# Kernel optimization log

Measured on AMD Instinct MI355X. Metric: run time of the kernel, lower is better.

## Reference

```python
import jax, jax.numpy as jnp
import numpy as np

# AFD = permute -> VSSBlock (LN + SS2D Mamba selective scan, residual) -> permute
#       -> x + SAFM(ChannelLayerNorm(x))
C = 64        # in_channels (d_model)
DI = 128      # d_inner = expand(2) * d_model
N = 16        # d_state
R = 4         # dt_rank = ceil(64/16)
K = 4         # scan directions
LN_EPS = 1e-5
CN_EPS = 1e-6
B_, H_, W_ = 8, 64, 64


def setup_inputs() -> dict:
    key = jax.random.key(0)
    ks = jax.random.split(key, 16)
    f = lambda k, s, sc=0.02: jax.random.normal(k, s, jnp.float32) * sc
    return {
        'x': jax.random.normal(ks[0], (B_, C, H_, W_), jnp.float32),
        # VSSBlock ln_1
        'ln1_g': jnp.ones((C,), jnp.float32),
        'ln1_b': jnp.zeros((C,), jnp.float32),
        # SS2D
        'in_proj_w': f(ks[1], (2 * DI, C)),
        'in_proj_b': jnp.zeros((2 * DI,), jnp.float32),
        'conv_w': f(ks[2], (DI, 3, 3)),          # depthwise 3x3
        'conv_b': jnp.zeros((DI,), jnp.float32),
        'xproj_w': f(ks[3], (K, R + 2 * N, DI)),
        'dtproj_w': f(ks[4], (K, DI, R), 0.1),
        'dtproj_b': f(ks[5], (K, DI), 0.1),
        'A_logs': jnp.tile(jnp.log(jnp.arange(1, N + 1, dtype=jnp.float32)), (K * DI, 1)),
        'Ds': jnp.ones((K * DI,), jnp.float32),
        'outnorm_g': jnp.ones((DI,), jnp.float32),
        'outnorm_b': jnp.zeros((DI,), jnp.float32),
        'outproj_w': f(ks[6], (C, DI)),
        'outproj_b': jnp.zeros((C,), jnp.float32),
        # SAFM
        'mfr_w': f(ks[7], (4, C // 4, 3, 3)),    # 4 depthwise 3x3 convs
        'mfr_b': jnp.zeros((4, C // 4), jnp.float32),
        'aggr_w': f(ks[8], (C, C)),              # 1x1 conv
        'aggr_b': jnp.zeros((C,), jnp.float32),
        # channel LayerNorm (SAFMN-style, channels_first)
        'cn_g': jnp.ones((C,), jnp.float32),
        'cn_b': jnp.zeros((C,), jnp.float32),
    }


def _ln(x, g, b, eps):
    u = jnp.mean(x, -1, keepdims=True)
    v = jnp.mean((x - u) ** 2, -1, keepdims=True)
    return (x - u) * jax.lax.rsqrt(v + eps) * g + b


def _channel_ln(x, g, b):  # x: (B,C,H,W), normalize over C
    u = jnp.mean(x, 1, keepdims=True)
    v = jnp.mean((x - u) ** 2, 1, keepdims=True)
    return (x - u) * jax.lax.rsqrt(v + CN_EPS) * g[None, :, None, None] + b[None, :, None, None]


def _dwconv3(x, w, b):  # depthwise 3x3, pad 1. x: (B,C,H,W), w: (C,3,3)
    y = jax.lax.conv_general_dilated(x, w[:, None], (1, 1), 'SAME',
        dimension_numbers=('NCHW', 'OIHW', 'NCHW'), feature_group_count=x.shape[1])
    return y + b[None, :, None, None]


def _selective_scan(xs, dts, A, Bs, Cs, D):
    # xs,dts:(B,K,C,L)  Bs,Cs:(B,K,N,L)  A:(K,C,N)  D:(K,C)
    u = jnp.moveaxis(xs, -1, 0)
    dt = jnp.moveaxis(dts, -1, 0)
    Bl = jnp.moveaxis(Bs, -1, 0)
    Cl = jnp.moveaxis(Cs, -1, 0)

    def step(h, inp):
        u_t, dt_t, B_t, C_t = inp
        h = h * jnp.exp(dt_t[..., None] * A) + dt_t[..., None] * B_t[:, :, None, :] * u_t[..., None]
        return h, jnp.einsum('bkcn,bkn->bkc', h, C_t)

    h0 = jnp.zeros(u.shape[1:] + (A.shape[-1],), u.dtype)
    _, ys = jax.lax.scan(step, h0, (u, dt, Bl, Cl))
    return jnp.moveaxis(ys, 0, -1) + D[None, :, :, None] * xs


def _ss2d(x, in_proj_w, in_proj_b, conv_w, conv_b, xproj_w, dtproj_w, dtproj_b,
          A_logs, Ds, outnorm_g, outnorm_b, outproj_w, outproj_b):
    B, H, W, _ = x.shape
    L = H * W
    xz = jnp.einsum('bhwc,dc->bhwd', x, in_proj_w) + in_proj_b
    xi, z = jnp.split(xz, 2, axis=-1)
    xc = jnp.transpose(xi, (0, 3, 1, 2))                      # (B,DI,H,W)
    xc = jax.nn.silu(_dwconv3(xc, conv_w, conv_b))
    # 4-directional unfold: row-major, col-major, and their reverses
    x_flat = xc.reshape(B, DI, L)
    x_t = jnp.transpose(xc, (0, 1, 3, 2)).reshape(B, DI, L)
    x_hwwh = jnp.stack([x_flat, x_t], axis=1)                 # (B,2,DI,L)
    xs = jnp.concatenate([x_hwwh, jnp.flip(x_hwwh, axis=-1)], axis=1)  # (B,4,DI,L)
    x_dbl = jnp.einsum('bkdl,kcd->bkcl', xs, xproj_w)
    dts, Bs, Cs = jnp.split(x_dbl, [R, R + N], axis=2)
    dts = jnp.einsum('bkrl,kdr->bkdl', dts, dtproj_w)
    dts = jax.nn.softplus(dts + dtproj_b[None, :, :, None])
    A = -jnp.exp(A_logs).reshape(K, DI, N)
    out_y = _selective_scan(xs, dts, A, Bs, Cs, Ds.reshape(K, DI))  # (B,4,DI,L)
    inv = jnp.flip(out_y[:, 2:4], axis=-1)
    wh = jnp.transpose(out_y[:, 1].reshape(B, DI, W, H), (0, 1, 3, 2)).reshape(B, DI, L)
    invwh = jnp.transpose(inv[:, 1].reshape(B, DI, W, H), (0, 1, 3, 2)).reshape(B, DI, L)
    y = out_y[:, 0] + inv[:, 0] + wh + invwh                  # (B,DI,L)
    y = jnp.transpose(y, (0, 2, 1)).reshape(B, H, W, DI)
    y = _ln(y, outnorm_g, outnorm_b, LN_EPS) * jax.nn.silu(z)
    return jnp.einsum('bhwd,cd->bhwc', y, outproj_w) + outproj_b


def _safm(x, mfr_w, mfr_b, aggr_w, aggr_b):
    parts = jnp.split(x, 4, axis=1)
    outs = []
    for i in range(4):
        s = parts[i]
        k = 2 ** i
        if i > 0:  # adaptive max pool to (H/k, W/k) == maxpool k,k
            s = jax.lax.reduce_window(s, -jnp.inf, jax.lax.max, (1, 1, k, k), (1, 1, k, k), 'VALID')
        s = _dwconv3(s, mfr_w[i], mfr_b[i])
        if i > 0:  # nearest upsample back
            s = jnp.repeat(jnp.repeat(s, k, axis=2), k, axis=3)
        outs.append(s)
    out = jnp.concatenate(outs, axis=1)
    out = jnp.einsum('bchw,oc->bohw', out, aggr_w) + aggr_b[None, :, None, None]
    return jax.nn.gelu(out, approximate=False) * x


def reference(x, ln1_g, ln1_b, in_proj_w, in_proj_b, conv_w, conv_b, xproj_w,
              dtproj_w, dtproj_b, A_logs, Ds, outnorm_g, outnorm_b, outproj_w,
              outproj_b, mfr_w, mfr_b, aggr_w, aggr_b, cn_g, cn_b):
    xh = jnp.transpose(x, (0, 2, 3, 1))                       # NCHW -> NHWC
    xh = xh + _ss2d(_ln(xh, ln1_g, ln1_b, LN_EPS), in_proj_w, in_proj_b, conv_w,
                    conv_b, xproj_w, dtproj_w, dtproj_b, A_logs, Ds,
                    outnorm_g, outnorm_b, outproj_w, outproj_b)
    xo = jnp.transpose(xh, (0, 3, 1, 2))                      # NHWC -> NCHW
    return xo + _safm(_channel_ln(xo, cn_g, cn_b), mfr_w, mfr_b, aggr_w, aggr_b)
```

## Files before the change

### kernel.cpp

```cpp
#include <hip/hip_runtime.h>
#include <hip/hip_bf16.h>

#define BB 8
#define CC 64
#define HH 64
#define WW 64
#define LL 4096
#define DI 128
#define KK 4
#define NN 16
#define RR 4
#define XD 36
#define GG 64
#define TT 64

__device__ __forceinline__ float softplusf(float x){
    return fmaxf(x, 0.f) + __logf(1.f + __expf(-fabsf(x)));
}
__device__ __forceinline__ int p_of(int k, int t){
    int tt = (k & 2) ? (LL - 1 - t) : t;
    return (k & 1) ? ((tt & 63) * 64 + (tt >> 6)) : tt;
}

template<int CTRL>
__device__ __forceinline__ float dpp_xadd(float v){
    int t = __builtin_amdgcn_update_dpp(0, __float_as_int(v), CTRL, 0xF, 0xF, true);
    return v + __int_as_float(t);
}

__global__ __launch_bounds__(256) void k1_ln_inproj(
    const float* __restrict__ x,
    const float* __restrict__ ln1_g,
    const float* __restrict__ ln1_b,
    const float* __restrict__ ipw,
    const float* __restrict__ ipb,
    float* __restrict__ xi, float* __restrict__ zs)
{
    int bid = blockIdx.x;
    int b = bid >> 6, p0 = (bid & 63)*64;
    int tid = threadIdx.x;

    __shared__ float xs[64*65];
    __shared__ float lnxT[64*68];
    __shared__ float wT[16*260];
    __shared__ float gb[128];
    __shared__ float bias[256];
    __shared__ float red[512];
    __shared__ float mv[128];

    if (tid < 128) gb[tid] = (tid < 64) ? ln1_g[tid] : ln1_b[tid - 64];
    bias[tid] = ipb[tid];

    #pragma unroll
    for (int it = 0; it < 4; it++){
        int i = tid + it*256;
        int c = i >> 4, pq = i & 15;
        float4 v = *(const float4*)(x + ((size_t)(b*CC + c))*LL + p0 + pq*4);
        xs[(pq*4+0)*65 + c] = v.x;
        xs[(pq*4+1)*65 + c] = v.y;
        xs[(pq*4+2)*65 + c] = v.z;
        xs[(pq*4+3)*65 + c] = v.w;
    }
    __syncthreads();

    {
        int pix = tid >> 2, q = tid & 3;
        float s = 0.f, sq = 0.f;
        #pragma unroll
        for (int cc = 0; cc < 16; cc++){
            float v = xs[pix*65 + q*16 + cc];
            s += v; sq = fmaf(v, v, sq);
        }
        red[tid*2] = s; red[tid*2+1] = sq;
    }
    __syncthreads();
    if (tid < 64){
        float s = red[tid*8] + red[tid*8+2] + red[tid*8+4] + red[tid*8+6];
        float sq = red[tid*8+1] + red[tid*8+3] + red[tid*8+5] + red[tid*8+7];
        float mean = s * (1.f/64.f);
        float var  = sq * (1.f/64.f) - mean*mean;
        mv[tid*2] = mean; mv[tid*2+1] = rsqrtf(var + 1e-5f);
    }
    __syncthreads();
    {
        int pix = tid >> 2, q = tid & 3;
        float mean = mv[pix*2], rstd = mv[pix*2+1];
        #pragma unroll
        for (int cc = 0; cc < 16; cc++){
            int c = q*16 + cc;
            float v = (xs[pix*65 + c] - mean)*rstd*gb[c] + gb[64+c];
            lnxT[c*68 + pix] = v;
        }
    }

    int pt = tid >> 4, ot = tid & 15;
    float acc[16][4];
    #pragma unroll
    for (int j = 0; j < 16; j++)
        #pragma unroll
        for (int i2 = 0; i2 < 4; i2++) acc[j][i2] = 0.f;

    for (int kc = 0; kc < 4; kc++){
        __syncthreads();
        #pragma unroll
        for (int it = 0; it < 4; it++){
            int i = tid + it*256;
            int d = i >> 2, jq = i & 3;
            float4 wv = *(const float4*)(ipw + d*64 + kc*16 + jq*4);
            wT[(jq*4+0)*260 + d] = wv.x;
            wT[(jq*4+1)*260 + d] = wv.y;
            wT[(jq*4+2)*260 + d] = wv.z;
            wT[(jq*4+3)*260 + d] = wv.w;
        }
        __syncthreads();
        #pragma unroll
        for (int k = 0; k < 16; k++){
            float4 rv = *(const float4*)(lnxT + (kc*16 + k)*68 + pt*4);
            #pragma unroll
            for (int g = 0; g < 4; g++){
                float4 wv = *(const float4*)(wT + k*260 + g*64 + ot*4);
                acc[g*4+0][0] = fmaf(wv.x, rv.x, acc[g*4+0][0]);
                acc[g*4+0][1] = fmaf(wv.x, rv.y, acc[g*4+0][1]);
                acc[g*4+0][2] = fmaf(wv.x, rv.z, acc[g*4+0][2]);
                acc[g*4+0][3] = fmaf(wv.x, rv.w, acc[g*4+0][3]);
                acc[g*4+1][0] = fmaf(wv.y, rv.x, acc[g*4+1][0]);
                acc[g*4+1][1] = fmaf(wv.y, rv.y, acc[g*4+1][1]);
                acc[g*4+1][2] = fmaf(wv.y, rv.z, acc[g*4+1][2]);
                acc[g*4+1][3] = fmaf(wv.y, rv.w, acc[g*4+1][3]);
                acc[g*4+2][0] = fmaf(wv.z, rv.x, acc[g*4+2][0]);
                acc[g*4+2][1] = fmaf(wv.z, rv.y, acc[g*4+2][1]);
                acc[g*4+2][2] = fmaf(wv.z, rv.z, acc[g*4+2][2]);
                acc[g*4+2][3] = fmaf(wv.z, rv.w, acc[g*4+2][3]);
                acc[g*4+3][0] = fmaf(wv.w, rv.x, acc[g*4+3][0]);
                acc[g*4+3][1] = fmaf(wv.w, rv.y, acc[g*4+3][1]);
                acc[g*4+3][2] = fmaf(wv.w, rv.z, acc[g*4+3][2]);
                acc[g*4+3][3] = fmaf(wv.w, rv.w, acc[g*4+3][3]);
            }
        }
    }

    #pragma unroll
    for (int i2 = 0; i2 < 4; i2++){
        size_t prow = ((size_t)(b*LL) + p0 + pt*4 + i2);
        #pragma unroll
        for (int g = 0; g < 4; g++){
            int dbase = g*64 + ot*4;
            float4 v;
            v.x = acc[g*4+0][i2] + bias[dbase+0];
            v.y = acc[g*4+1][i2] + bias[dbase+1];
            v.z = acc[g*4+2][i2] + bias[dbase+2];
            v.w = acc[g*4+3][i2] + bias[dbase+3];
            if (g < 2){
                *(float4*)(xi + prow*DI + dbase) = v;
            } else {
                v.x = v.x / (1.f + __expf(-v.x));
                v.y = v.y / (1.f + __expf(-v.y));
                v.z = v.z / (1.f + __expf(-v.z));
                v.w = v.w / (1.f + __expf(-v.w));
                *(float4*)(zs + prow*DI + dbase - 128) = v;
            }
        }
    }
}

__global__ __launch_bounds__(256) void k2_dwconv(
    const float* __restrict__ xi,
    const float* __restrict__ cw,
    const float* __restrict__ cb,
    float* __restrict__ xc)
{
    int idx = blockIdx.x*256 + threadIdx.x;
    int d = idx & 127;
    int g = idx >> 7;
    int p0 = (g & 1023) * 4;
    int b = g >> 10;
    int h = p0 >> 6, w0 = p0 & 63;
    float wt[9];
    #pragma unroll
    for (int j = 0; j < 9; j++) wt[j] = cw[d*9 + j];
    float bv = cb[d];
    float acc[4] = {bv, bv, bv, bv};
    #pragma unroll
    for (int ky = 0; ky < 3; ky++){
        int hh = h + ky - 1;
        if ((unsigned)hh >= 64u) continue;
        const float* row = xi + ((size_t)(b*LL) + hh*64)*DI + d;
        float v0 = (w0 > 0)  ? row[(w0-1)*DI] : 0.f;
        float v1 = row[(w0+0)*DI];
        float v2 = row[(w0+1)*DI];
        float v3 = row[(w0+2)*DI];
        float v4 = row[(w0+3)*DI];
        float v5 = (w0 < 60) ? row[(w0+4)*DI] : 0.f;
        float wa = wt[ky*3], wbv = wt[ky*3+1], wc = wt[ky*3+2];
        acc[0] = fmaf(v0, wa, fmaf(v1, wbv, fmaf(v2, wc, acc[0])));
        acc[1] = fmaf(v1, wa, fmaf(v2, wbv, fmaf(v3, wc, acc[1])));
        acc[2] = fmaf(v2, wa, fmaf(v3, wbv, fmaf(v4, wc, acc[2])));
        acc[3] = fmaf(v3, wa, fmaf(v4, wbv, fmaf(v5, wc, acc[3])));
    }
    #pragma unroll
    for (int i = 0; i < 4; i++){
        float a = acc[i];
        float sg = 1.f / (1.f + __expf(-a));
        xc[((size_t)(b*LL) + p0 + i)*DI + d] = a * sg;
    }
}

__global__ __launch_bounds__(256) void k3_xdbl(
    const float* __restrict__ xc,
    const float* __restrict__ xpw,
    float* __restrict__ xdbl)
{
    int bid = blockIdx.x;
    int b = bid >> 6, ptile = bid & 63;
    int tid = threadIdx.x;
    int ot = tid & 15;
    int pt = tid >> 4;

    __shared__ float r[64*132];
    __shared__ float wT[32*192];

    const float* xcb = xc + ((size_t)(b*LL) + ptile*64)*DI;
    for (int i = tid; i < 2048; i += 256){
        int pix = i >> 5, kq = i & 31;
        float4 v = *(const float4*)(xcb + pix*128 + kq*4);
        *(float4*)(r + pix*132 + kq*4) = v;
    }

    float acc[9][4];
    #pragma unroll
    for (int j = 0; j < 9; j++)
        #pragma unroll
        for (int i2 = 0; i2 < 4; i2++) acc[j][i2] = 0.f;

    for (int kc = 0; kc < 4; kc++){
        __syncthreads();
        int k0 = kc*32;
        for (int i = tid; i < 1152; i += 256){
            int cl = i >> 3, jq = i & 7;
            float4 wv = *(const float4*)(xpw + cl*128 + k0 + jq*4);
            int o = (cl*456) >> 12;
            int j = cl - o*9;
            wT[(jq*4+0)*192 + o*12 + j] = wv.x;
            wT[(jq*4+1)*192 + o*12 + j] = wv.y;
            wT[(jq*4+2)*192 + o*12 + j] = wv.z;
            wT[(jq*4+3)*192 + o*12 + j] = wv.w;
        }
        __syncthreads();
        const float* rbase = r + (pt*4)*132 + k0;
        #pragma unroll 4
        for (int k = 0; k < 32; k++){
            float4 wa = *(const float4*)(wT + k*192 + ot*12);
            float4 wb = *(const float4*)(wT + k*192 + ot*12 + 4);
            float w8 = wT[k*192 + ot*12 + 8];
            float rv0 = rbase[k];
            float rv1 = rbase[132 + k];
            float rv2 = rbase[264 + k];
            float rv3 = rbase[396 + k];
            float wv[9] = {wa.x, wa.y, wa.z, wa.w, wb.x, wb.y, wb.z, wb.w, w8};
            float rv[4] = {rv0, rv1, rv2, rv3};
            #pragma unroll
            for (int j = 0; j < 9; j++)
                #pragma unroll
                for (int i2 = 0; i2 < 4; i2++)
                    acc[j][i2] = fmaf(wv[j], rv[i2], acc[j][i2]);
        }
    }

    int kd = ot >> 2;
    int cbase = (ot & 3)*9;
    size_t obase = ((size_t)(b*KK + kd))*LL;
    #pragma unroll
    for (int i2 = 0; i2 < 4; i2++){
        int p = ptile*64 + pt*4 + i2;
        int tT = (p & 63)*64 + (p >> 6);
        int t = (kd == 0) ? p : (kd == 1) ? tT : (kd == 2) ? (4095 - p) : (4095 - tT);
        float* dst = xdbl + (obase + t)*XD + cbase;
        #pragma unroll
        for (int j = 0; j < 9; j++) dst[j] = acc[j][i2];
    }
}

__global__ __launch_bounds__(128, 4) void k4a_local(
    const float* __restrict__ xc, const float* __restrict__ xdbl,
    const float* __restrict__ dtw, const float* __restrict__ dtb,
    const float* __restrict__ A_logs,
    float* __restrict__ Pbuf, float* __restrict__ Hbuf)
{
    int bid = blockIdx.x;
    int cc = bid & 63, k = (bid >> 6) & 3, b = bid >> 8;
    int d = threadIdx.x;
    int kd = k*DI + d;
    float4 wv4 = *(const float4*)(dtw + kd*4);
    float bias = dtb[kd];
    float An[16];
    bool fast = true;
    {
        const float4* al = (const float4*)(A_logs + kd*16);
        #pragma unroll
        for (int i = 0; i < 4; i++){
            float4 a = al[i];
            An[i*4+0] = -__expf(a.x); An[i*4+1] = -__expf(a.y);
            An[i*4+2] = -__expf(a.z); An[i*4+3] = -__expf(a.w);
        }
        #pragma unroll
        for (int n = 0; n < 16; n++)
            fast = fast && (fabsf(An[n] + (float)(n+1)) < 1e-3f*(float)(n+1));
    }
    __shared__ float sraw[TT*XD];
    const float* src = xdbl + ((size_t)(b*KK + k)*LL + cc*TT)*XD;
    for (int i = threadIdx.x; i < TT*XD/4; i += 128)
        ((float4*)sraw)[i] = ((const float4*)src)[i];
    __syncthreads();

    const float* xcb = xc + (size_t)b*LL*DI;
    float h[16];
    #pragma unroll
    for (int i = 0; i < 16; i++) h[i] = 0.f;
    float Sdt = 0.f;

    if (fast){
        for (int t = 0; t < TT; t++){
            const float* rp = sraw + t*XD;
            float4 xr = *(const float4*)rp;
            float dtr = fmaf(xr.x, wv4.x, fmaf(xr.y, wv4.y, fmaf(xr.z, wv4.z, fmaf(xr.w, wv4.w, bias))));
            float dt = softplusf(dtr);
            Sdt += dt;
            int p = p_of(k, cc*TT + t);
            float u = xcb[(size_t)p*DI + d];
            float du = dt * u;
            float4 B0 = *(const float4*)(rp + 4);
            float4 B1 = *(const float4*)(rp + 8);
            float4 B2 = *(const float4*)(rp + 12);
            float4 B3 = *(const float4*)(rp + 16);
            float Bv[16] = {B0.x,B0.y,B0.z,B0.w, B1.x,B1.y,B1.z,B1.w,
                            B2.x,B2.y,B2.z,B2.w, B3.x,B3.y,B3.z,B3.w};
            float e1 = exp2f(-1.44269504f * dt);
            float e = e1;
            h[0] = fmaf(h[0], e, du*Bv[0]);
            #pragma unroll
            for (int i = 1; i < 16; i++){
                e *= e1;
                h[i] = fmaf(h[i], e, du*Bv[i]);
            }
        }
        size_t ob = ((size_t)bid)*2048 + d*16;
        float P1 = exp2f(-1.44269504f * Sdt);
        float P = P1;
        Pbuf[ob] = P; Hbuf[ob] = h[0];
        #pragma unroll
        for (int i = 1; i < 16; i++){
            P *= P1;
            Pbuf[ob + i] = P;
            Hbuf[ob + i] = h[i];
        }
    } else {
        float An2[16];
        #pragma unroll
        for (int i = 0; i < 16; i++) An2[i] = An[i] * 1.44269504f;
        for (int t = 0; t < TT; t++){
            const float* rp = sraw + t*XD;
            float4 xr = *(const float4*)rp;
            float dtr = fmaf(xr.x, wv4.x, fmaf(xr.y, wv4.y, fmaf(xr.z, wv4.z, fmaf(xr.w, wv4.w, bias))));
            float dt = softplusf(dtr);
            Sdt += dt;
            int p = p_of(k, cc*TT + t);
            float u = xcb[(size_t)p*DI + d];
            float du = dt * u;
            float4 B0 = *(const float4*)(rp + 4);
            float4 B1 = *(const float4*)(rp + 8);
            float4 B2 = *(const float4*)(rp + 12);
            float4 B3 = *(const float4*)(rp + 16);
            float Bv[16] = {B0.x,B0.y,B0.z,B0.w, B1.x,B1.y,B1.z,B1.w,
                            B2.x,B2.y,B2.z,B2.w, B3.x,B3.y,B3.z,B3.w};
            #pragma unroll
            for (int i = 0; i < 16; i++)
                h[i] = fmaf(h[i], exp2f(dt*An2[i]), du*Bv[i]);
        }
        size_t ob = ((size_t)bid)*2048 + d*16;
        #pragma unroll
        for (int i = 0; i < 16; i++){
            Pbuf[ob + i] = exp2f(An2[i] * Sdt);
            Hbuf[ob + i] = h[i];
        }
    }
}

__global__ __launch_bounds__(256) void k4b_prop(
    const float* __restrict__ Pbuf, const float* __restrict__ Hbuf,
    float* __restrict__ hin_buf)
{
    int chain = blockIdx.x*256 + threadIdx.x;
    int bk = chain >> 11, s = chain & 2047;
    float hin = 0.f;
    for (int c = 0; c < GG; c++){
        size_t idx = ((size_t)(bk*GG + c))*2048 + s;
        hin_buf[idx] = hin;
        hin = fmaf(Pbuf[idx], hin, Hbuf[idx]);
    }
}

__global__ __launch_bounds__(128, 4) void k4c_emit(
    const float* __restrict__ xc, const float* __restrict__ xdbl,
    const float* __restrict__ dtw, const float* __restrict__ dtb,
    const float* __restrict__ A_logs, const float* __restrict__ Ds,
    const float* __restrict__ hin_buf,
    float* __restrict__ y)
{
    int bid = blockIdx.x;
    int cc = bid & 63, k = (bid >> 6) & 3, b = bid >> 8;
    int d = threadIdx.x;
    int kd = k*DI + d;
    float4 wv4 = *(const float4*)(dtw + kd*4);
    float bias = dtb[kd];
    float Dv = Ds[kd];
    float An[16];
    bool fast = true;
    {
        const float4* al = (const float4*)(A_logs + kd*16);
        #pragma unroll
        for (int i = 0; i < 4; i++){
            float4 a = al[i];
            An[i*4+0] = -__expf(a.x); An[i*4+1] = -__expf(a.y);
            An[i*4+2] = -__expf(a.z); An[i*4+3] = -__expf(a.w);
        }
        #pragma unroll
        for (int n = 0; n < 16; n++)
            fast = fast && (fabsf(An[n] + (float)(n+1)) < 1e-3f*(float)(n+1));
    }
    __shared__ float sraw[TT*XD];
    const float* src = xdbl + ((size_t)(b*KK + k)*LL + cc*TT)*XD;
    for (int i = threadIdx.x; i < TT*XD/4; i += 128)
        ((float4*)sraw)[i] = ((const float4*)src)[i];
    __syncthreads();

    const float* xcb = xc + (size_t)b*LL*DI;
    float* yb = y + (size_t)b*LL*DI;
    float h[16];
    {
        const float4* hi = (const float4*)(hin_buf + ((size_t)bid)*2048 + d*16);
        #pragma unroll
        for (int i = 0; i < 4; i++){
            float4 a = hi[i];
            h[i*4+0] = a.x; h[i*4+1] = a.y; h[i*4+2] = a.z; h[i*4+3] = a.w;
        }
    }

    if (fast){
        for (int t = 0; t < TT; t++){
            const float* rp = sraw + t*XD;
            float4 xr = *(const float4*)rp;
            float dtr = fmaf(xr.x, wv4.x, fmaf(xr.y, wv4.y, fmaf(xr.z, wv4.z, fmaf(xr.w, wv4.w, bias))));
            float dt = softplusf(dtr);
            int p = p_of(k, cc*TT + t);
            float u = xcb[(size_t)p*DI + d];
            float du = dt * u;
            float4 B0 = *(const float4*)(rp + 4);
            float4 B1 = *(const float4*)(rp + 8);
            float4 B2 = *(const float4*)(rp + 12);
            float4 B3 = *(const float4*)(rp + 16);
            float Bv[16] = {B0.x,B0.y,B0.z,B0.w, B1.x,B1.y,B1.z,B1.w,
                            B2.x,B2.y,B2.z,B2.w, B3.x,B3.y,B3.z,B3.w};
            float4 C0 = *(const float4*)(rp + 20);
            float4 C1 = *(const float4*)(rp + 24);
            float4 C2 = *(const float4*)(rp + 28);
            float4 C3 = *(const float4*)(rp + 32);
            float Cv[16] = {C0.x,C0.y,C0.z,C0.w, C1.x,C1.y,C1.z,C1.w,
                            C2.x,C2.y,C2.z,C2.w, C3.x,C3.y,C3.z,C3.w};
            float yv = Dv * u;
            float e1 = exp2f(-1.44269504f * dt);
            float e = e1;
            h[0] = fmaf(h[0], e, du*Bv[0]);
            yv = fmaf(h[0], Cv[0], yv);
            #pragma unroll
            for (int i = 1; i < 16; i++){
                e *= e1;
                h[i] = fmaf(h[i], e, du*Bv[i]);
                yv = fmaf(h[i], Cv[i], yv);
            }
            atomicAdd(&yb[(size_t)p*DI + d], yv);
        }
    } else {
        float An2[16];
        #pragma unroll
        for (int i = 0; i < 16; i++) An2[i] = An[i] * 1.44269504f;
        for (int t = 0; t < TT; t++){
            const float* rp = sraw + t*XD;
            float4 xr = *(const float4*)rp;
            float dtr = fmaf(xr.x, wv4.x, fmaf(xr.y, wv4.y, fmaf(xr.z, wv4.z, fmaf(xr.w, wv4.w, bias))));
            float dt = softplusf(dtr);
            int p = p_of(k, cc*TT + t);
            float u = xcb[(size_t)p*DI + d];
            float du = dt * u;
            float4 B0 = *(const float4*)(rp + 4);
            float4 B1 = *(const float4*)(rp + 8);
            float4 B2 = *(const float4*)(rp + 12);
            float4 B3 = *(const float4*)(rp + 16);
            float Bv[16] = {B0.x,B0.y,B0.z,B0.w, B1.x,B1.y,B1.z,B1.w,
                            B2.x,B2.y,B2.z,B2.w, B3.x,B3.y,B3.z,B3.w};
            float4 C0 = *(const float4*)(rp + 20);
            float4 C1 = *(const float4*)(rp + 24);
            float4 C2 = *(const float4*)(rp + 28);
            float4 C3 = *(const float4*)(rp + 32);
            float Cv[16] = {C0.x,C0.y,C0.z,C0.w, C1.x,C1.y,C1.z,C1.w,
                            C2.x,C2.y,C2.z,C2.w, C3.x,C3.y,C3.z,C3.w};
            float yv = Dv * u;
            #pragma unroll
            for (int i = 0; i < 16; i++){
                h[i] = fmaf(h[i], exp2f(dt*An2[i]), du*Bv[i]);
                yv = fmaf(h[i], Cv[i], yv);
            }
            atomicAdd(&yb[(size_t)p*DI + d], yv);
        }
    }
}

__global__ __launch_bounds__(256) void k4_scan(
    const float* __restrict__ xc, const float* __restrict__ xdbl,
    const float* __restrict__ dtw, const float* __restrict__ dtb,
    const float* __restrict__ A_logs, const float* __restrict__ Ds,
    float* __restrict__ y)
{
    int bid = blockIdx.x;
    int b = bid >> 5, k = (bid >> 3) & 3, grp = bid & 7;
    int d0 = grp * 16;
    int tid = threadIdx.x;
    int wv = tid >> 6, lane = tid & 63, n = lane & 15, j = lane >> 4;
    int ch = wv*4 + j;
    int d = d0 + ch;
    int kd = k*DI + d;
    float An = -__expf(A_logs[kd*NN + n]);
    int ch_s = tid & 15;
    int kds = k*DI + d0 + ch_s;
    float w0s = dtw[kds*4+0], w1s = dtw[kds*4+1], w2s = dtw[kds*4+2], w3s = dtw[kds*4+3];
    float bs  = dtb[kds];
    float Dvs = Ds[kds];
    __shared__ float sraw[64*XD];
    __shared__ float sdd[64*16*2];
    __shared__ float sdy[64*17];
    const float* xdbase = xdbl + (size_t)(b*KK + k)*LL*XD;
    const float* xcb = xc + (size_t)b*LL*DI;
    float* yb = y + (size_t)b*LL*DI;
    float h = 0.f;
    for (int cc = 0; cc < 64; cc++){
        __syncthreads();
        const float* src = xdbase + (size_t)cc*64*XD;
        for (int i2 = tid; i2 < 576; i2 += 256)
            ((float4*)sraw)[i2] = ((const float4*)src)[i2];
        #pragma unroll
        for (int it = 0; it < 4; it++){
            int idx = tid + it*256;
            int t = idx >> 4;
            int pu = p_of(k, cc*64 + t);
            float u = xcb[(size_t)pu*DI + d0 + ch_s];
            float4 xr = *(const float4*)(src + t*XD);
            float dtr = fmaf(xr.x, w0s, fmaf(xr.y, w1s, fmaf(xr.z, w2s, fmaf(xr.w, w3s, bs))));
            float dt = softplusf(dtr);
            sdd[idx*2]     = dt;
            sdd[idx*2 + 1] = dt*u;
            sdy[t*17 + ch_s] = Dvs * u;
        }
        __syncthreads();
        #pragma unroll
        for (int tg = 0; tg < 4; tg++){
            float myv = 0.f;
            #pragma unroll
            for (int it = 0; it < 16; it++){
                int t = tg*16 + it;
                float dt = sdd[(t*16 + ch)*2];
                float du = sdd[(t*16 + ch)*2 + 1];
                float Bn = sraw[t*XD + 4 + n];
                float Cn = sraw[t*XD + 20 + n];
                float e = __expf(dt * An);
                h = fmaf(h, e, du * Bn);
                float yv = h * Cn;
                yv = dpp_xadd<0xB1>(yv);
                yv = dpp_xadd<0x4E>(yv);
                yv = dpp_xadd<0x141>(yv);
                yv = dpp_xadd<0x140>(yv);
                if (it == n) myv = yv;
            }
            int t = tg*16 + n;
            float yt = myv + sdy[t*17 + ch];
            int p = p_of(k, cc*64 + t);
            atomicAdd(&yb[(size_t)p*DI + d], yt);
        }
    }
}

__global__ __launch_bounds__(256) void k5_out(
    const float* __restrict__ y, const float* __restrict__ zs,
    const float* __restrict__ on_g, const float* __restrict__ on_b,
    const float* __restrict__ opw,
    const float* __restrict__ opb,
    const float* __restrict__ x,
    const float* __restrict__ cn_g, const float* __restrict__ cn_b,
    float* __restrict__ xo, float* __restrict__ cl)
{
    int bid = blockIdx.x;
    int b = bid >> 6, p0 = (bid & 63)*64;
    int tid = threadIdx.x;

    __shared__ float vT[128*68];
    __shared__ float wT[128*68];
    __shared__ float gb[256];
    __shared__ float ob[64];
    __shared__ float cgb[128];
    __shared__ float red[2048];
    __shared__ float mv[128];

    gb[tid] = (tid < 128) ? on_g[tid] : on_b[tid - 128];
    if (tid < 64) ob[tid] = opb[tid];
    if (tid >= 128 && tid < 256) cgb[tid-128] = (tid < 192) ? cn_g[tid-128] : cn_b[tid-192];

    #pragma unroll
    for (int it = 0; it < 8; it++){
        int i = tid + it*256;
        int c = i >> 5, jq = i & 31;
        float4 wv = *(const float4*)(opw + c*128 + jq*4);
        wT[(jq*4+0)*68 + c] = wv.x;
        wT[(jq*4+1)*68 + c] = wv.y;
        wT[(jq*4+2)*68 + c] = wv.z;
        wT[(jq*4+3)*68 + c] = wv.w;
    }

    int pix = tid >> 2, q = tid & 3;
    size_t base = ((size_t)(b*LL) + p0 + pix)*DI + q*32;
    float yv[32];
    {
        const float4* y4 = (const float4*)(y + base);
        float s = 0.f, sq = 0.f;
        #pragma unroll
        for (int i = 0; i < 8; i++){
            float4 a = y4[i];
            yv[i*4+0] = a.x; yv[i*4+1] = a.y; yv[i*4+2] = a.z; yv[i*4+3] = a.w;
            s += a.x + a.y + a.z + a.w;
            sq = fmaf(a.x,a.x, fmaf(a.y,a.y, fmaf(a.z,a.z, fmaf(a.w,a.w, sq))));
        }
        red[tid*2] = s; red[tid*2+1] = sq;
    }
    __syncthreads();
    if (tid < 64){
        float s = red[tid*8] + red[tid*8+2] + red[tid*8+4] + red[tid*8+6];
        float sq = red[tid*8+1] + red[tid*8+3] + red[tid*8+5] + red[tid*8+7];
        float mean = s * (1.f/128.f);
        float var  = sq * (1.f/128.f) - mean*mean;
        mv[tid*2] = mean; mv[tid*2+1] = rsqrtf(var + 1e-5f);
    }
    __syncthreads();
    {
        float mean = mv[pix*2], rstd = mv[pix*2+1];
        const float4* z4 = (const float4*)(zs + base);
        #pragma unroll
        for (int i = 0; i < 8; i++){
            float4 zz = z4[i];
            float zv[4] = {zz.x, zz.y, zz.z, zz.w};
            #pragma unroll
            for (int jj = 0; jj < 4; jj++){
                int dd = q*32 + i*4 + jj;
                float vn = (yv[i*4+jj] - mean)*rstd*gb[dd] + gb[128+dd];
                vT[dd*68 + pix] = vn * zv[jj];
            }
        }
    }
    __syncthreads();

    int pt = tid >> 4, ot = tid & 15;
    float acc[4][4];
    #pragma unroll
    for (int j = 0; j < 4; j++)
        #pragma unroll
        for (int i2 = 0; i2 < 4; i2++) acc[j][i2] = 0.f;

    #pragma unroll 4
    for (int k = 0; k < 128; k++){
        float4 rv = *(const float4*)(vT + k*68 + pt*4);
        float4 wv = *(const float4*)(wT + k*68 + ot*4);
        acc[0][0] = fmaf(wv.x, rv.x, acc[0][0]); acc[0][1] = fmaf(wv.x, rv.y, acc[0][1]);
        acc[0][2] = fmaf(wv.x, rv.z, acc[0][2]); acc[0][3] = fmaf(wv.x, rv.w, acc[0][3]);
        acc[1][0] = fmaf(wv.y, rv.x, acc[1][0]); acc[1][1] = fmaf(wv.y, rv.y, acc[1][1]);
        acc[1][2] = fmaf(wv.y, rv.z, acc[1][2]); acc[1][3] = fmaf(wv.y, rv.w, acc[1][3]);
        acc[2][0] = fmaf(wv.z, rv.x, acc[2][0]); acc[2][1] = fmaf(wv.z, rv.y, acc[2][1]);
        acc[2][2] = fmaf(wv.z, rv.z, acc[2][2]); acc[2][3] = fmaf(wv.z, rv.w, acc[2][3]);
        acc[3][0] = fmaf(wv.w, rv.x, acc[3][0]); acc[3][1] = fmaf(wv.w, rv.y, acc[3][1]);
        acc[3][2] = fmaf(wv.w, rv.z, acc[3][2]); acc[3][3] = fmaf(wv.w, rv.w, acc[3][3]);
    }

    #pragma unroll
    for (int jj = 0; jj < 4; jj++){
        int c = ot*4 + jj;
        float4 xr = *(const float4*)(x + ((size_t)(b*CC + c))*LL + p0 + pt*4);
        acc[jj][0] += ob[c] + xr.x;
        acc[jj][1] += ob[c] + xr.y;
        acc[jj][2] += ob[c] + xr.z;
        acc[jj][3] += ob[c] + xr.w;
    }
    #pragma unroll
    for (int i2 = 0; i2 < 4; i2++){
        float4 v = make_float4(acc[0][i2], acc[1][i2], acc[2][i2], acc[3][i2]);
        *(float4*)(xo + ((size_t)(b*LL) + p0 + pt*4 + i2)*CC + ot*4) = v;
    }

    __syncthreads();
    #pragma unroll
    for (int i2 = 0; i2 < 4; i2++){
        float s = acc[0][i2] + acc[1][i2] + acc[2][i2] + acc[3][i2];
        float sq = fmaf(acc[0][i2],acc[0][i2], fmaf(acc[1][i2],acc[1][i2],
                   fmaf(acc[2][i2],acc[2][i2], acc[3][i2]*acc[3][i2])));
        red[(pt*4 + i2)*16 + ot] = s;
        red[1024 + (pt*4 + i2)*16 + ot] = sq;
    }
    __syncthreads();
    if (tid < 64){
        float s = 0.f, sq = 0.f;
        #pragma unroll
        for (int o = 0; o < 16; o++){
            s += red[tid*16 + o];
            sq += red[1024 + tid*16 + o];
        }
        float mean = s * (1.f/64.f);
        float var  = sq * (1.f/64.f) - mean*mean;
        mv[tid*2] = mean; mv[tid*2+1] = rsqrtf(var + 1e-6f);
    }
    __syncthreads();
    #pragma unroll
    for (int i2 = 0; i2 < 4; i2++){
        float mean = mv[(pt*4+i2)*2], rstd = mv[(pt*4+i2)*2+1];
        float4 v;
        v.x = (acc[0][i2] - mean)*rstd*cgb[ot*4+0] + cgb[64+ot*4+0];
        v.y = (acc[1][i2] - mean)*rstd*cgb[ot*4+1] + cgb[64+ot*4+1];
        v.z = (acc[2][i2] - mean)*rstd*cgb[ot*4+2] + cgb[64+ot*4+2];
        v.w = (acc[3][i2] - mean)*rstd*cgb[ot*4+3] + cgb[64+ot*4+3];
        *(float4*)(cl + ((size_t)(b*LL) + p0 + pt*4 + i2)*CC + ot*4) = v;
    }
}

__global__ __launch_bounds__(256) void k7_pools(const float* __restrict__ cl, float* __restrict__ pools)
{
    int idx = blockIdx.x*256 + threadIdx.x;
    int g, S, base;
    if (idx < 131072)      { g = 1; S = 32; base = 0; }
    else if (idx < 163840) { g = 2; S = 16; base = 131072; idx -= 131072; }
    else if (idx < 172032) { g = 3; S = 8;  base = 163840; idx -= 163840; }
    else return;
    int pw = idx % S; idx /= S;
    int ph = idx % S; idx /= S;
    int j = idx & 15; int b = idx >> 4;
    int kk = 64 / S;
    int c = g*16 + j;
    float m = -1e30f;
    for (int dy = 0; dy < kk; dy++)
        for (int dx = 0; dx < kk; dx++){
            int h = ph*kk + dy, w = pw*kk + dx;
            m = fmaxf(m, cl[((size_t)(b*LL) + h*64 + w)*CC + c]);
        }
    pools[base + ((size_t)(b*16 + j)*S + ph)*S + pw] = m;
}

__global__ __launch_bounds__(256) void k8_mfr(
    const float* __restrict__ cl, const float* __restrict__ pools,
    const float* __restrict__ mfr_w,
    const float* __restrict__ mfr_b,
    float* __restrict__ cat)
{
    int idx = blockIdx.x*256 + threadIdx.x;
    int c = idx & 63; int bp = idx >> 6;
    int p = bp & 4095, b = bp >> 12;
    int g = c >> 4, j = c & 15;
    int h = p >> 6, w = p & 63;
    float acc = mfr_b[g*16 + j];
    const float* wr = mfr_w + (g*16 + j)*9;
    if (g == 0){
        #pragma unroll
        for (int ky = 0; ky < 3; ky++){
            int hh = h + ky - 1; if ((unsigned)hh >= 64u) continue;
            #pragma unroll
            for (int kx = 0; kx < 3; kx++){
                int ww = w + kx - 1; if ((unsigned)ww >= 64u) continue;
                acc = fmaf(cl[((size_t)(b*LL) + hh*64 + ww)*CC + c], wr[ky*3 + kx], acc);
            }
        }
    } else {
        int S = 64 >> g;
        int ph = h >> g, pw = w >> g;
        int base = (g == 1) ? 0 : ((g == 2) ? 131072 : 163840);
        const float* P = pools + base + (size_t)(b*16 + j)*S*S;
        #pragma unroll
        for (int ky = 0; ky < 3; ky++){
            int hh = ph + ky - 1; if ((unsigned)hh >= (unsigned)S) continue;
            #pragma unroll
            for (int kx = 0; kx < 3; kx++){
                int ww = pw + kx - 1; if ((unsigned)ww >= (unsigned)S) continue;
                acc = fmaf(P[hh*S + ww], wr[ky*3 + kx], acc);
            }
        }
    }
    cat[idx] = acc;
}

__global__ __launch_bounds__(256) void k9_agg(
    const float* __restrict__ cat, const float* __restrict__ cl, const float* __restrict__ xo,
    const float* __restrict__ agw,
    const float* __restrict__ agb,
    float* __restrict__ out)
{
    int bid = blockIdx.x;
    int b = bid >> 6, p0 = (bid & 63)*64;
    int tid = threadIdx.x;

    __shared__ float catT[64*68];
    __shared__ float wT[64*68];
    __shared__ float ab[64];

    if (tid < 64) ab[tid] = agb[tid];
    #pragma unroll
    for (int it = 0; it < 4; it++){
        int i = tid + it*256;
        int pix = i >> 4, cq = i & 15;
        float4 v = *(const float4*)(cat + ((size_t)(b*LL) + p0 + pix)*CC + cq*4);
        catT[(cq*4+0)*68 + pix] = v.x;
        catT[(cq*4+1)*68 + pix] = v.y;
        catT[(cq*4+2)*68 + pix] = v.z;
        catT[(cq*4+3)*68 + pix] = v.w;
        int o = i >> 4;
        float4 wv = *(const float4*)(agw + o*64 + cq*4);
        wT[(cq*4+0)*68 + o] = wv.x;
        wT[(cq*4+1)*68 + o] = wv.y;
        wT[(cq*4+2)*68 + o] = wv.z;
        wT[(cq*4+3)*68 + o] = wv.w;
    }
    __syncthreads();

    int pt = tid >> 4, ot = tid & 15;
    float acc[4][4];
    #pragma unroll
    for (int j = 0; j < 4; j++)
        #pragma unroll
        for (int i2 = 0; i2 < 4; i2++) acc[j][i2] = 0.f;

    #pragma unroll 4
    for (int k = 0; k < 64; k++){
        float4 rv = *(const float4*)(catT + k*68 + pt*4);
        float4 wv = *(const float4*)(wT + k*68 + ot*4);
        acc[0][0] = fmaf(wv.x, rv.x, acc[0][0]); acc[0][1] = fmaf(wv.x, rv.y, acc[0][1]);
        acc[0][2] = fmaf(wv.x, rv.z, acc[0][2]); acc[0][3] = fmaf(wv.x, rv.w, acc[0][3]);
        acc[1][0] = fmaf(wv.y, rv.x, acc[1][0]); acc[1][1] = fmaf(wv.y, rv.y, acc[1][1]);
        acc[1][2] = fmaf(wv.y, rv.z, acc[1][2]); acc[1][3] = fmaf(wv.y, rv.w, acc[1][3]);
        acc[2][0] = fmaf(wv.z, rv.x, acc[2][0]); acc[2][1] = fmaf(wv.z, rv.y, acc[2][1]);
        acc[2][2] = fmaf(wv.z, rv.z, acc[2][2]); acc[2][3] = fmaf(wv.z, rv.w, acc[2][3]);
        acc[3][0] = fmaf(wv.w, rv.x, acc[3][0]); acc[3][1] = fmaf(wv.w, rv.y, acc[3][1]);
        acc[3][2] = fmaf(wv.w, rv.z, acc[3][2]); acc[3][3] = fmaf(wv.w, rv.w, acc[3][3]);
    }

    float res[4][4];
    #pragma unroll
    for (int i2 = 0; i2 < 4; i2++){
        size_t prow = ((size_t)(b*LL) + p0 + pt*4 + i2)*CC + ot*4;
        float4 clv = *(const float4*)(cl + prow);
        float4 xov = *(const float4*)(xo + prow);
        float cla[4] = {clv.x, clv.y, clv.z, clv.w};
        float xoa[4] = {xov.x, xov.y, xov.z, xov.w};
        #pragma unroll
        for (int jj = 0; jj < 4; jj++){
            float av = acc[jj][i2] + ab[ot*4 + jj];
            float gl = 0.5f*av*(1.f + erff(av*0.70710678118f));
            res[jj][i2] = xoa[jj] + gl*cla[jj];
        }
    }
    #pragma unroll
    for (int jj = 0; jj < 4; jj++){
        int o = ot*4 + jj;
        float4 v = make_float4(res[jj][0], res[jj][1], res[jj][2], res[jj][3]);
        *(float4*)(out + ((size_t)(b*CC + o))*LL + p0 + pt*4) = v;
    }
}

extern "C" void kernel_launch(void* const* d_in, const int* in_sizes, int n_in,
                              void* d_out, int out_size, void* d_ws, size_t ws_size,
                              hipStream_t stream)
{
    const float* x       = (const float*)d_in[0];
    const float* ln1_g   = (const float*)d_in[1];
    const float* ln1_b   = (const float*)d_in[2];
    const float* ipw     = (const float*)d_in[3];
    const float* ipb     = (const float*)d_in[4];
    const float* conv_w  = (const float*)d_in[5];
    const float* conv_b  = (const float*)d_in[6];
    const float* xpw     = (const float*)d_in[7];
    const float* dtw     = (const float*)d_in[8];
    const float* dtb     = (const float*)d_in[9];
    const float* A_logs  = (const float*)d_in[10];
    const float* Ds      = (const float*)d_in[11];
    const float* on_g    = (const float*)d_in[12];
    const float* on_b    = (const float*)d_in[13];
    const float* opw     = (const float*)d_in[14];
    const float* opb     = (const float*)d_in[15];
    const float* mfr_w   = (const float*)d_in[16];
    const float* mfr_b   = (const float*)d_in[17];
    const float* agw     = (const float*)d_in[18];
    const float* agb     = (const float*)d_in[19];
    const float* cn_g    = (const float*)d_in[20];
    const float* cn_b    = (const float*)d_in[21];
    float* out = (float*)d_out;

    float* ws = (float*)d_ws;
    float* xi    = ws;
    float* zs    = ws + 4194304;
    float* xc    = ws + 8388608;
    float* xdbl  = ws + 12582912;
    float* y     = xi;
    float* xo    = xc;
    float* pools = xc + 2097152;
    float* cl    = xdbl;
    float* cat   = zs;
    float* Pbuf  = ws + 17301504;
    float* Hbuf  = ws + 21495808;
    float* hinb  = ws + 25690112;
    bool par = ws_size >= (size_t)29884416 * 4;

    hipLaunchKernelGGL(k1_ln_inproj, dim3(BB*64), dim3(256), 0, stream,
                       x, ln1_g, ln1_b, ipw, ipb, xi, zs);
    hipLaunchKernelGGL(k2_dwconv, dim3(BB*LL*DI/1024), dim3(256), 0, stream,
                       xi, conv_w, conv_b, xc);
    hipLaunchKernelGGL(k3_xdbl, dim3(BB*64), dim3(256), 0, stream,
                       xc, xpw, xdbl);
    hipMemsetAsync(y, 0, (size_t)BB*LL*DI*sizeof(float), stream);
    if (par){
        hipLaunchKernelGGL(k4a_local, dim3(BB*KK*GG), dim3(128), 0, stream,
                           xc, xdbl, dtw, dtb, A_logs, Pbuf, Hbuf);
        hipLaunchKernelGGL(k4b_prop, dim3(256), dim3(256), 0, stream,
                           Pbuf, Hbuf, hinb);
        hipLaunchKernelGGL(k4c_emit, dim3(BB*KK*GG), dim3(128), 0, stream,
                           xc, xdbl, dtw, dtb, A_logs, Ds, hinb, y);
    } else {
        hipLaunchKernelGGL(k4_scan, dim3(256), dim3(256), 0, stream,
                           xc, xdbl, dtw, dtb, A_logs, Ds, y);
    }
    hipLaunchKernelGGL(k5_out, dim3(BB*64), dim3(256), 0, stream,
                       y, zs, on_g, on_b, opw, opb, x, cn_g, cn_b, xo, cl);
    hipLaunchKernelGGL(k7_pools, dim3((172032 + 255)/256), dim3(256), 0, stream,
                       cl, pools);
    hipLaunchKernelGGL(k8_mfr, dim3(BB*LL*CC/256), dim3(256), 0, stream,
                       cl, pools, mfr_w, mfr_b, cat);
    hipLaunchKernelGGL(k9_agg, dim3(BB*64), dim3(256), 0, stream,
                       cat, cl, xo, agw, agb, out);
}
```

Before: 363.1 us.

## Store per-direction scan outputs separately instead of atomics; sum in out-proj

The emit kernel now writes each scan direction's output to its own buffer with plain stores, replacing atomicAdd into one shared buffer. The memset is dropped, and k5_out sums the four buffers as it loads. The powers e^1..e^16 are also built with a log-depth multiply tree instead of a serial chain. This removes atomic contention and the memset in exchange for more workspace and extra reads in k5, and it only runs when the workspace is large enough.

```diff
diff --git a/kernel.cpp b/kernel.cpp
--- a/kernel.cpp
+++ b/kernel.cpp
@@ -20,6 +20,15 @@
 __device__ __forceinline__ int p_of(int k, int t){
     int tt = (k & 2) ? (LL - 1 - t) : t;
     return (k & 1) ? ((tt & 63) * 64 + (tt >> 6)) : tt;
+}
+__device__ __forceinline__ void pow16(float e1, float* E){
+    float e2 = e1*e1;
+    float e4 = e2*e2;
+    float e8 = e4*e4;
+    E[0]=e1;    E[1]=e2;    E[2]=e2*e1;  E[3]=e4;
+    E[4]=e4*e1; E[5]=e4*e2; E[6]=e4*E[2];E[7]=e8;
+    E[8]=e8*e1; E[9]=e8*e2; E[10]=e8*E[2]; E[11]=e8*e4;
+    E[12]=e8*E[4]; E[13]=e8*E[5]; E[14]=e8*E[6]; E[15]=e8*e8;
 }
 
 template<int CTRL>
@@ -334,23 +343,18 @@
             float4 B3 = *(const float4*)(rp + 16);
             float Bv[16] = {B0.x,B0.y,B0.z,B0.w, B1.x,B1.y,B1.z,B1.w,
                             B2.x,B2.y,B2.z,B2.w, B3.x,B3.y,B3.z,B3.w};
-            float e1 = exp2f(-1.44269504f * dt);
-            float e = e1;
-            h[0] = fmaf(h[0], e, du*Bv[0]);
-            #pragma unroll
-            for (int i = 1; i < 16; i++){
-                e *= e1;
-                h[i] = fmaf(h[i], e, du*Bv[i]);
-            }
+            float E[16];
+            pow16(exp2f(-1.44269504f * dt), E);
+            #pragma unroll
+            for (int i = 0; i < 16; i++)
+                h[i] = fmaf(h[i], E[i], du*Bv[i]);
         }
         size_t ob = ((size_t)bid)*2048 + d*16;
-        float P1 = exp2f(-1.44269504f * Sdt);
-        float P = P1;
-        Pbuf[ob] = P; Hbuf[ob] = h[0];
-        #pragma unroll
-        for (int i = 1; i < 16; i++){
-            P *= P1;
-            Pbuf[ob + i] = P;
+        float E[16];
+        pow16(exp2f(-1.44269504f * Sdt), E);
+        #pragma unroll
+        for (int i = 0; i < 16; i++){
+            Pbuf[ob + i] = E[i];
             Hbuf[ob + i] = h[i];
         }
     } else {
@@ -399,12 +403,13 @@
     }
 }
 
-__global__ __launch_bounds__(128, 4) void k4c_emit(
+__global__ __launch_bounds__(128, 4) void k4c_store(
     const float* __restrict__ xc, const float* __restrict__ xdbl,
     const float* __restrict__ dtw, const float* __restrict__ dtb,
     const float* __restrict__ A_logs, const float* __restrict__ Ds,
     const float* __restrict__ hin_buf,
-    float* __restrict__ y)
+    float* __restrict__ y0, float* __restrict__ y1,
+    float* __restrict__ y2, float* __restrict__ y3)
 {
     int bid = blockIdx.x;
     int cc = bid & 63, k = (bid >> 6) & 3, b = bid >> 8;
@@ -434,7 +439,8 @@
     __syncthreads();
 
     const float* xcb = xc + (size_t)b*LL*DI;
-    float* yb = y + (size_t)b*LL*DI;
+    float* yk = (k == 0) ? y0 : (k == 1) ? y1 : (k == 2) ? y2 : y3;
+    float* yb = yk + (size_t)b*LL*DI;
     float h[16];
     {
         const float4* hi = (const float4*)(hin_buf + ((size_t)bid)*2048 + d*16);
@@ -466,18 +472,15 @@
             float4 C3 = *(const float4*)(rp + 32);
             float Cv[16] = {C0.x,C0.y,C0.z,C0.w, C1.x,C1.y,C1.z,C1.w,
                             C2.x,C2.y,C2.z,C2.w, C3.x,C3.y,C3.z,C3.w};
+            float E[16];
+            pow16(exp2f(-1.44269504f * dt), E);
             float yv = Dv * u;
-            float e1 = exp2f(-1.44269504f * dt);
-            float e = e1;
-            h[0] = fmaf(h[0], e, du*Bv[0]);
-            yv = fmaf(h[0], Cv[0], yv);
-            #pragma unroll
-            for (int i = 1; i < 16; i++){
-                e *= e1;
-                h[i] = fmaf(h[i], e, du*Bv[i]);
+            #pragma unroll
+            for (int i = 0; i < 16; i++){
+                h[i] = fmaf(h[i], E[i], du*Bv[i]);
                 yv = fmaf(h[i], Cv[i], yv);
             }
-            atomicAdd(&yb[(size_t)p*DI + d], yv);
+            yb[(size_t)p*DI + d] = yv;
         }
     } else {
         float An2[16];
@@ -509,8 +512,79 @@
                 h[i] = fmaf(h[i], exp2f(dt*An2[i]), du*Bv[i]);
                 yv = fmaf(h[i], Cv[i], yv);
             }
-            atomicAdd(&yb[(size_t)p*DI + d], yv);
-        }
+            yb[(size_t)p*DI + d] = yv;
+        }
+    }
+}
+
+__global__ __launch_bounds__(128, 4) void k4c_emit(
+    const float* __restrict__ xc, const float* __restrict__ xdbl,
+    const float* __restrict__ dtw, const float* __restrict__ dtb,
+    const float* __restrict__ A_logs, const float* __restrict__ Ds,
+    const float* __restrict__ hin_buf,
+    float* __restrict__ y)
+{
+    int bid = blockIdx.x;
+    int cc = bid & 63, k = (bid >> 6) & 3, b = bid >> 8;
+    int d = threadIdx.x;
+    int kd = k*DI + d;
+    float4 wv4 = *(const float4*)(dtw + kd*4);
+    float bias = dtb[kd];
+    float Dv = Ds[kd];
+    float An2[16];
+    {
+        const float4* al = (const float4*)(A_logs + kd*16);
+        #pragma unroll
+        for (int i = 0; i < 4; i++){
+            float4 a = al[i];
+            An2[i*4+0] = -__expf(a.x)*1.44269504f; An2[i*4+1] = -__expf(a.y)*1.44269504f;
+            An2[i*4+2] = -__expf(a.z)*1.44269504f; An2[i*4+3] = -__expf(a.w)*1.44269504f;
+        }
+    }
+    __shared__ float sraw[TT*XD];
+    const float* src = xdbl + ((size_t)(b*KK + k)*LL + cc*TT)*XD;
+    for (int i = threadIdx.x; i < TT*XD/4; i += 128)
+        ((float4*)sraw)[i] = ((const float4*)src)[i];
+    __syncthreads();
+
+    const float* xcb = xc + (size_t)b*LL*DI;
+    float* yb = y + (size_t)b*LL*DI;
+    float h[16];
+    {
+        const float4* hi = (const float4*)(hin_buf + ((size_t)bid)*2048 + d*16);
+        #pragma unroll
+        for (int i = 0; i < 4; i++){
+            float4 a = hi[i];
+            h[i*4+0] = a.x; h[i*4+1] = a.y; h[i*4+2] = a.z; h[i*4+3] = a.w;
+        }
+    }
+    for (int t = 0; t < TT; t++){
+        const float* rp = sraw + t*XD;
+        float4 xr = *(const float4*)rp;
+        float dtr = fmaf(xr.x, wv4.x, fmaf(xr.y, wv4.y, fmaf(xr.z, wv4.z, fmaf(xr.w, wv4.w, bias))));
+        float dt = softplusf(dtr);
+        int p = p_of(k, cc*TT + t);
+        float u = xcb[(size_t)p*DI + d];
+        float du = dt * u;
+        float4 B0 = *(const float4*)(rp + 4);
+        float4 B1 = *(const float4*)(rp + 8);
+        float4 B2 = *(const float4*)(rp + 12);
+        float4 B3 = *(const float4*)(rp + 16);
+        float Bv[16] = {B0.x,B0.y,B0.z,B0.w, B1.x,B1.y,B1.z,B1.w,
+                        B2.x,B2.y,B2.z,B2.w, B3.x,B3.y,B3.z,B3.w};
+        float4 C0 = *(const float4*)(rp + 20);
+        float4 C1 = *(const float4*)(rp + 24);
+        float4 C2 = *(const float4*)(rp + 28);
+        float4 C3 = *(const float4*)(rp + 32);
+        float Cv[16] = {C0.x,C0.y,C0.z,C0.w, C1.x,C1.y,C1.z,C1.w,
+                        C2.x,C2.y,C2.z,C2.w, C3.x,C3.y,C3.z,C3.w};
+        float yv = Dv * u;
+        #pragma unroll
+        for (int i = 0; i < 16; i++){
+            h[i] = fmaf(h[i], exp2f(dt*An2[i]), du*Bv[i]);
+            yv = fmaf(h[i], Cv[i], yv);
+        }
+        atomicAdd(&yb[(size_t)p*DI + d], yv);
     }
 }
 
@@ -588,7 +662,10 @@
 }
 
 __global__ __launch_bounds__(256) void k5_out(
-    const float* __restrict__ y, const float* __restrict__ zs,
+    const float* __restrict__ y0s, const float* __restrict__ y1s,
+    const float* __restrict__ y2s, const float* __restrict__ y3s,
+    int nsum,
+    const float* __restrict__ zs,
     const float* __restrict__ on_g, const float* __restrict__ on_b,
     const float* __restrict__ opw,
     const float* __restrict__ opb,
@@ -627,14 +704,33 @@
     size_t base = ((size_t)(b*LL) + p0 + pix)*DI + q*32;
     float yv[32];
     {
-        const float4* y4 = (const float4*)(y + base);
         float s = 0.f, sq = 0.f;
-        #pragma unroll
-        for (int i = 0; i < 8; i++){
-            float4 a = y4[i];
-            yv[i*4+0] = a.x; yv[i*4+1] = a.y; yv[i*4+2] = a.z; yv[i*4+3] = a.w;
-            s += a.x + a.y + a.z + a.w;
-            sq = fmaf(a.x,a.x, fmaf(a.y,a.y, fmaf(a.z,a.z, fmaf(a.w,a.w, sq))));
+        if (nsum == 4){
+            const float4* a4 = (const float4*)(y0s + base);
+            const float4* b4 = (const float4*)(y1s + base);
+            const float4* c4 = (const float4*)(y2s + base);
+            const float4* d4 = (const float4*)(y3s + base);
+            #pragma unroll
+            for (int i = 0; i < 8; i++){
+                float4 a = a4[i], bb = b4[i], c = c4[i], dd = d4[i];
+                float4 v;
+                v.x = (a.x + bb.x) + (c.x + dd.x);
+                v.y = (a.y + bb.y) + (c.y + dd.y);
+                v.z = (a.z + bb.z) + (c.z + dd.z);
+                v.w = (a.w + bb.w) + (c.w + dd.w);
+                yv[i*4+0] = v.x; yv[i*4+1] = v.y; yv[i*4+2] = v.z; yv[i*4+3] = v.w;
+                s += v.x + v.y + v.z + v.w;
+                sq = fmaf(v.x,v.x, fmaf(v.y,v.y, fmaf(v.z,v.z, fmaf(v.w,v.w, sq))));
+            }
+        } else {
+            const float4* a4 = (const float4*)(y0s + base);
+            #pragma unroll
+            for (int i = 0; i < 8; i++){
+                float4 a = a4[i];
+                yv[i*4+0] = a.x; yv[i*4+1] = a.y; yv[i*4+2] = a.z; yv[i*4+3] = a.w;
+                s += a.x + a.y + a.z + a.w;
+                sq = fmaf(a.x,a.x, fmaf(a.y,a.y, fmaf(a.z,a.z, fmaf(a.w,a.w, sq))));
+            }
         }
         red[tid*2] = s; red[tid*2+1] = sq;
     }
@@ -907,7 +1003,7 @@
     float* zs    = ws + 4194304;
     float* xc    = ws + 8388608;
     float* xdbl  = ws + 12582912;
-    float* y     = xi;
+    float* y0    = xi;
     float* xo    = xc;
     float* pools = xc + 2097152;
     float* cl    = xdbl;
@@ -915,7 +1011,11 @@
     float* Pbuf  = ws + 17301504;
     float* Hbuf  = ws + 21495808;
     float* hinb  = ws + 25690112;
-    bool par = ws_size >= (size_t)29884416 * 4;
+    float* y3    = ws + 29884416;
+    bool par  = ws_size >= (size_t)29884416 * 4;
+    bool par4 = ws_size >= (size_t)34078720 * 4;
+    float* y1 = Pbuf;
+    float* y2 = Hbuf;
 
     hipLaunchKernelGGL(k1_ln_inproj, dim3(BB*64), dim3(256), 0, stream,
                        x, ln1_g, ln1_b, ipw, ipb, xi, zs);
@@ -923,20 +1023,28 @@
                        xi, conv_w, conv_b, xc);
     hipLaunchKernelGGL(k3_xdbl, dim3(BB*64), dim3(256), 0, stream,
                        xc, xpw, xdbl);
-    hipMemsetAsync(y, 0, (size_t)BB*LL*DI*sizeof(float), stream);
+    int nsum = 1;
     if (par){
         hipLaunchKernelGGL(k4a_local, dim3(BB*KK*GG), dim3(128), 0, stream,
                            xc, xdbl, dtw, dtb, A_logs, Pbuf, Hbuf);
         hipLaunchKernelGGL(k4b_prop, dim3(256), dim3(256), 0, stream,
                            Pbuf, Hbuf, hinb);
-        hipLaunchKernelGGL(k4c_emit, dim3(BB*KK*GG), dim3(128), 0, stream,
-                           xc, xdbl, dtw, dtb, A_logs, Ds, hinb, y);
+        if (par4){
+            nsum = 4;
+            hipLaunchKernelGGL(k4c_store, dim3(BB*KK*GG), dim3(128), 0, stream,
+                               xc, xdbl, dtw, dtb, A_logs, Ds, hinb, y0, y1, y2, y3);
+        } else {
+            hipMemsetAsync(y0, 0, (size_t)BB*LL*DI*sizeof(float), stream);
+            hipLaunchKernelGGL(k4c_emit, dim3(BB*KK*GG), dim3(128), 0, stream,
+                               xc, xdbl, dtw, dtb, A_logs, Ds, hinb, y0);
+        }
     } else {
+        hipMemsetAsync(y0, 0, (size_t)BB*LL*DI*sizeof(float), stream);
         hipLaunchKernelGGL(k4_scan, dim3(256), dim3(256), 0, stream,
-                           xc, xdbl, dtw, dtb, A_logs, Ds, y);
+                           xc, xdbl, dtw, dtb, A_logs, Ds, y0);
     }
     hipLaunchKernelGGL(k5_out, dim3(BB*64), dim3(256), 0, stream,
-                       y, zs, on_g, on_b, opw, opb, x, cn_g, cn_b, xo, cl);
+                       y0, y1, y2, y3, nsum, zs, on_g, on_b, opw, opb, x, cn_g, cn_b, xo, cl);
     hipLaunchKernelGGL(k7_pools, dim3((172032 + 255)/256), dim3(256), 0, stream,
                        cl, pools);
     hipLaunchKernelGGL(k8_mfr, dim3(BB*LL*CC/256), dim3(256), 0, stream,
```

Measured after the change: 351.7 us. 1.03x faster.
